# Kernel optimization log

Measured on AMD Instinct MI355X. Metric: run time of the kernel, lower is better.

Reference implementation:

```python
import jax, jax.numpy as jnp
import numpy as np

B, T, C, L = 256, 512, 128, 64  # batch, timesteps, num_classes (blank=C-1), max label len
NEG = -1e30  # finite -inf surrogate (avoids nan in grads)


def setup_inputs() -> dict:
    key = jax.random.key(0)
    k1, k2, k3, k4 = jax.random.split(key, 4)
    logits = jax.random.normal(k1, (B, T, C), dtype=jnp.float32)
    y_pred = jax.nn.softmax(logits, axis=-1)  # ctc_batch_cost expects softmax probs
    y_true = jax.random.randint(k2, (B, L), 0, C - 1, dtype=jnp.int32)  # non-blank labels
    input_length = jax.random.randint(k3, (B, 1), T // 2, T + 1, dtype=jnp.int32)
    label_length = jax.random.randint(k4, (B, 1), L // 2, L + 1, dtype=jnp.int32)
    return {"y_true": y_true, "y_pred": y_pred,
            "input_length": input_length, "label_length": label_length}


def _ctc_loss(log_probs, labels, input_length, label_length, blank):
    # log_probs: [B,T,C]; labels: [B,L]; lengths: [B]
    b, t_max, _ = log_probs.shape
    l_max = labels.shape[1]
    s_max = 2 * l_max + 1
    # extended label sequence: blank, l1, blank, l2, ..., blank  -> [B,S]
    ext = jnp.full((b, s_max), blank, dtype=labels.dtype)
    ext = ext.at[:, 1::2].set(labels)
    # gathered log probs per extended symbol: [B,T,S]
    lp = jnp.take_along_axis(log_probs, ext[:, None, :].astype(jnp.int32), axis=2)
    # skip (s-2 -> s) allowed where ext[s] != blank and ext[s] != ext[s-2]
    skip = jnp.zeros((b, s_max), dtype=bool)
    skip = skip.at[:, 2:].set((ext[:, 2:] != blank) & (ext[:, 2:] != ext[:, :-2]))
    # init alpha at t=0: only s=0 (blank) and s=1 (first label) reachable
    alpha0 = jnp.full((b, s_max), NEG, dtype=log_probs.dtype)
    alpha0 = alpha0.at[:, 0].set(lp[:, 0, 0])
    alpha0 = alpha0.at[:, 1].set(lp[:, 0, 1])
    in_len = input_length

    def step(alpha, inp):
        lp_t, t = inp  # lp_t: [B,S]
        s1 = jnp.pad(alpha, ((0, 0), (1, 0)), constant_values=NEG)[:, :-1]
        s2 = jnp.pad(alpha, ((0, 0), (2, 0)), constant_values=NEG)[:, :-2]
        a = jnp.logaddexp(alpha, s1)
        a = jnp.where(skip, jnp.logaddexp(a, s2), a)
        new = a + lp_t
        new = jnp.where((t < in_len)[:, None], new, alpha)  # freeze past input_length
        return new, None

    lp_time_major = jnp.swapaxes(lp, 0, 1)  # [T,B,S]
    ts = jnp.arange(1, t_max)
    alpha, _ = jax.lax.scan(step, alpha0, (lp_time_major[1:], ts))
    lab = label_length
    idx_last = 2 * lab  # final blank position; idx_last-1 is final label position
    a_last = jnp.take_along_axis(alpha, idx_last[:, None], axis=1)[:, 0]
    a_prev = jnp.take_along_axis(alpha, (idx_last - 1)[:, None], axis=1)[:, 0]
    return -jnp.logaddexp(a_last, a_prev)  # [B]


def reference(y_true, y_pred, input_length, label_length):
    eps = 1e-7  # keras epsilon added before log
    log_probs = jnp.log(y_pred + eps)
    blank = y_pred.shape[-1] - 1  # keras ctc_batch_cost blank convention
    loss = _ctc_loss(log_probs, y_true, input_length[:, 0], label_length[:, 0], blank)
    return loss[:, None]  # [B,1], matching tf expand_dims(ctc_loss, 1)
```

## Files before the change

### kernel.cpp

```cpp
#include <hip/hip_runtime.h>


#define B_ 256
#define T_ 512
#define C_ 128
#define L_ 64
#define BLANK_ 127
#define EPSF (1e-7f)
#define CHUNK 32
#define QSTR 36
#define LN2F 0.6931471805599453f

#define EXP2(x) __builtin_amdgcn_exp2f(x)
#define LOG2(x) __builtin_amdgcn_logf(x)

__device__ __forceinline__ float lse2_2(float a, float b) {
    float m = fmaxf(a, b);
    float d = fminf(a, b) - m;
    return m + LOG2(1.0f + EXP2(d));
}

__device__ __forceinline__ float dppf(float x) {
    return __int_as_float(__builtin_amdgcn_update_dpp(
        0, __float_as_int(x), 0x138, 0xf, 0xf, false));
}
__device__ __forceinline__ int dppi(int x) {
    return __builtin_amdgcn_update_dpp(0, x, 0x138, 0xf, 0xf, false);
}

__device__ __forceinline__ void stage_chunk(const float* gsrc, float* ldst, int lane) {
#pragma unroll
    for (int i = 0; i < CHUNK / 2; ++i) {
        __builtin_amdgcn_global_load_lds(
            (const __attribute__((address_space(1))) void*)(gsrc + i * 256 + lane * 4),
            (__attribute__((address_space(3))) void*)(ldst + i * 256),
            16, 0, 0);
    }
}

__device__ __forceinline__ void produce_chunk(const float* __restrict__ rk,
        float* __restrict__ qd, int lane, int label, int t0, int tend, float& llg)
{
    const float pbv  = rk[(lane & 31) * C_ + BLANK_] + EPSF;
    const float rpb  = 0.5f / pbv;
    const float erpb = EPSF * rpb;
    const int t = t0 + lane;
    const bool lgv = (lane < 32) && (t >= 1) && (t < tend);
    llg += lgv ? LOG2(pbv) : 0.0f;
#pragma unroll
    for (int k = 0; k < 8; ++k) {
        float q[4];
#pragma unroll
        for (int j = 0; j < 4; ++j) {
            const int r = 4 * k + j;
            const float pl = rk[r * C_ + label];
            const float rb = __int_as_float(
                __builtin_amdgcn_readlane(__float_as_int(rpb), r));
            const float eb = __int_as_float(
                __builtin_amdgcn_readlane(__float_as_int(erpb), r));
            q[j] = fmaf(pl, rb, eb);
        }
        *reinterpret_cast<float4*>(qd + lane * QSTR + 4 * k) =
            make_float4(q[0], q[1], q[2], q[3]);
    }
}

template<bool HAS128>
__device__ __forceinline__ void maybe_renorm(float& A0, float& A1, float& A2,
                                             int& e, float& sch) {
    float m2 = fmaxf(A0, A1);
    if (HAS128) m2 = fmaxf(m2, A2);
    const bool out = (m2 > 16777216.0f) ||
                     ((m2 < 5.9604644775390625e-8f) && (m2 > 0.0f));
    if (__any(out)) {
        const float mm = (m2 == 0.0f) ? 1.0f : m2;
        const int eb = __float_as_int(mm) >> 23;
        const float s = __int_as_float((254 - eb) << 23);
        A0 *= s; A1 *= s;
        if (HAS128) A2 *= s;
        e += eb - 127;
        const int ep = dppi(e);
        int d = ep - e;
        d = d < -125 ? -125 : d;
        d = d > 127 ? 127 : d;
        sch = __int_as_float((d + 126) << 23);
    }
}

template<bool HAS128>
__device__ __forceinline__ void step(float& A0, float& A1, float& A2,
                                     float sch, float skipf2, float ql) {
    const float P1 = dppf(A1) * sch;
    const float A0o = A0, A1o = A1;
    A0 = fmaf(A0o, 0.5f, P1);
    const float t = fmaf(skipf2, P1, A0o);
    A1 = (A1o + t) * ql;
    if (HAS128) A2 = (A2 + A1o) * 0.5f;
}

template<bool HAS128>
__device__ __forceinline__ void consumer(const float (*qlbuf)[64 * QSTR],
        const float* extra, int lane, int label, int lab, int tend, int nmax,
        float* out, int b)
{
    const int lprev = __shfl_up(label, 1);
    const float skipf2 = (lane > 0 && label != lprev) ? 2.0f : 0.0f;

    float A0 = 0.0f, A1 = 0.0f, A2 = 0.0f, sch = 0.5f;
    int e = 0;

    for (int c = 0; c < nmax; ++c) {
        const float* qb = &qlbuf[c & 1][lane * QSTR];
        float qlv[32];
#pragma unroll
        for (int k = 0; k < 8; ++k) {
            const float4 t4 = *reinterpret_cast<const float4*>(qb + 4 * k);
            qlv[4*k+0] = t4.x; qlv[4*k+1] = t4.y;
            qlv[4*k+2] = t4.z; qlv[4*k+3] = t4.w;
        }
        asm volatile("s_waitcnt lgkmcnt(0)" ::: "memory");
        __builtin_amdgcn_s_barrier();
        __builtin_amdgcn_sched_barrier(0);

        const int rem = tend - c * CHUNK;
        if (c == 0) {
            A0 = (lane == 0) ? extra[1] : 0.0f;
            A1 = (lane == 0) ? extra[0] : 0.0f;
#pragma unroll
            for (int u = 1; u < 32; ++u) {
                step<HAS128>(A0, A1, A2, sch, skipf2, qlv[u]);
                if ((u & 3) == 3) maybe_renorm<HAS128>(A0, A1, A2, e, sch);
            }
        } else if (rem >= CHUNK) {
#pragma unroll
            for (int u = 0; u < 32; ++u) {
                step<HAS128>(A0, A1, A2, sch, skipf2, qlv[u]);
                if ((u & 3) == 3) maybe_renorm<HAS128>(A0, A1, A2, e, sch);
            }
        } else {
            for (int u = 0; u < rem; ++u) {
                step<HAS128>(A0, A1, A2, sch, skipf2, qlv[u]);
                if ((u & 3) == 3) maybe_renorm<HAS128>(A0, A1, A2, e, sch);
            }
        }
    }
    __builtin_amdgcn_s_barrier();
    const float lg = extra[2];
    const float ef = (float)e + lg + (float)(tend - 1);
    const float l0 = LOG2(A0) + ef;
    const float l1 = LOG2(A1) + ef;
    const float a_prev = __shfl(l1, lab - 1);
    float a_last;
    if (HAS128) {
        const float l2 = LOG2(A2) + ef;
        a_last = __shfl(l2, 63);
    } else {
        a_last = __shfl(l0, lab);
    }
    if (lane == 0) out[b] = -LN2F * lse2_2(a_last, a_prev);
}

__global__ __launch_bounds__(128) void ctc_fwd_kernel(
    const int* __restrict__ y_true, const float* __restrict__ y_pred,
    const int* __restrict__ input_len, const int* __restrict__ label_len,
    float* __restrict__ out)
{
    __shared__ __align__(16) float raw[2][CHUNK * C_];
    __shared__ __align__(16) float qlbuf[2][64 * QSTR];
    __shared__ float extra[4];

    const int b = blockIdx.x;
    const int tid = threadIdx.x;
    const int lane = tid & 63;
    const float* __restrict__ Pg = y_pred + (size_t)b * T_ * C_;
    const int label = y_true[b * L_ + lane];
    const int in_len = input_len[b];
    const int tend = in_len < T_ ? in_len : T_;
    const int nmax = (tend + CHUNK - 1) / CHUNK;

    if (tid >= 64) {
        float llg = 0.0f;
        stage_chunk(Pg, &raw[0][0], lane);
        stage_chunk(Pg + CHUNK * C_, &raw[1][0], lane);
        asm volatile("s_waitcnt vmcnt(16)" ::: "memory");
        produce_chunk(&raw[0][0], &qlbuf[0][0], lane, label, 0, tend, llg);
        if (lane == 0) {
            extra[0] = raw[0][label] + EPSF;
            extra[1] = raw[0][BLANK_] + EPSF;
        }
        asm volatile("s_waitcnt lgkmcnt(0)" ::: "memory");
        __builtin_amdgcn_s_barrier();
        for (int c = 0; c < nmax; ++c) {
            if (c + 2 < nmax)
                stage_chunk(Pg + (size_t)(c + 2) * CHUNK * C_, &raw[c & 1][0], lane);
            if (c + 1 < nmax) {
                if (c + 2 < nmax) asm volatile("s_waitcnt vmcnt(16)" ::: "memory");
                else              asm volatile("s_waitcnt vmcnt(0)" ::: "memory");
                produce_chunk(&raw[(c + 1) & 1][0], &qlbuf[(c + 1) & 1][0],
                              lane, label, (c + 1) * CHUNK, tend, llg);
            }
            asm volatile("s_waitcnt lgkmcnt(0)" ::: "memory");
            __builtin_amdgcn_s_barrier();
        }
#pragma unroll
        for (int off = 16; off >= 1; off >>= 1) llg += __shfl_xor(llg, off);
        if (lane == 0) extra[2] = llg;
        asm volatile("s_waitcnt lgkmcnt(0)" ::: "memory");
        __builtin_amdgcn_s_barrier();
    } else {
        const int lab = label_len[b];
        __builtin_amdgcn_s_barrier();
        if (lab == L_) consumer<true >(qlbuf, extra, lane, label, lab, tend, nmax, out, b);
        else           consumer<false>(qlbuf, extra, lane, label, lab, tend, nmax, out, b);
    }
}

extern "C" void kernel_launch(void* const* d_in, const int* in_sizes, int n_in,
                              void* d_out, int out_size, void* d_ws, size_t ws_size,
                              hipStream_t stream) {
    const int*   y_true    = (const int*)d_in[0];
    const float* y_pred    = (const float*)d_in[1];
    const int*   input_len = (const int*)d_in[2];
    const int*   label_len = (const int*)d_in[3];
    float* out = (float*)d_out;

    ctc_fwd_kernel<<<B_, 128, 0, stream>>>(y_true, y_pred, input_len, label_len, out);
}
```

Before: 24.33 us.

## Split CTC recursion into concurrent forward-alpha and backward-beta halves

Each batch block now runs four waves: a forward producer and consumer computing alpha over the first half of the time steps, and a backward producer and consumer computing beta over the second half. The halves are joined by a log-sum-exp of alpha times beta across lanes. This halves the serial recurrence length, which is the latency-bound critical path per block. In exchange it doubles the waves and LDS per block, adds a reverse-time data layout and a combine step, and risks numerical or indexing errors at the split point and in the backward renormalisation.

```diff
diff --git a/kernel.cpp b/kernel.cpp
--- a/kernel.cpp
+++ b/kernel.cpp
@@ -8,8 +8,10 @@
 #define BLANK_ 127
 #define EPSF (1e-7f)
 #define CHUNK 32
-#define QSTR 36
+#define QSTRF 36
+#define QSTRB 68
 #define LN2F 0.6931471805599453f
+#define NEGF (-1e30f)
 
 #define EXP2(x) __builtin_amdgcn_exp2f(x)
 #define LOG2(x) __builtin_amdgcn_logf(x)
@@ -19,16 +21,25 @@
     float d = fminf(a, b) - m;
     return m + LOG2(1.0f + EXP2(d));
 }
-
-__device__ __forceinline__ float dppf(float x) {
+__device__ __forceinline__ float dppf_shr(float x) {
     return __int_as_float(__builtin_amdgcn_update_dpp(
         0, __float_as_int(x), 0x138, 0xf, 0xf, false));
 }
-__device__ __forceinline__ int dppi(int x) {
+__device__ __forceinline__ int dppi_shr(int x) {
     return __builtin_amdgcn_update_dpp(0, x, 0x138, 0xf, 0xf, false);
 }
-
-__device__ __forceinline__ void stage_chunk(const float* gsrc, float* ldst, int lane) {
+__device__ __forceinline__ float dppf_shl(float x) {
+    return __int_as_float(__builtin_amdgcn_update_dpp(
+        0, __float_as_int(x), 0x130, 0xf, 0xf, false));
+}
+__device__ __forceinline__ int dppi_shl(int x) {
+    return __builtin_amdgcn_update_dpp(0, x, 0x130, 0xf, 0xf, false);
+}
+__device__ __forceinline__ float rdlanef(float x, int i) {
+    return __int_as_float(__builtin_amdgcn_readlane(__float_as_int(x), i));
+}
+
+__device__ __forceinline__ void stage_rows(const float* gsrc, float* ldst, int lane) {
 #pragma unroll
     for (int i = 0; i < CHUNK / 2; ++i) {
         __builtin_amdgcn_global_load_lds(
@@ -38,15 +49,14 @@
     }
 }
 
-__device__ __forceinline__ void produce_chunk(const float* __restrict__ rk,
-        float* __restrict__ qd, int lane, int label, int t0, int tend, float& llg)
+__device__ __forceinline__ void produce_fwd(const float* __restrict__ rk,
+        float* __restrict__ qd, int lane, int label, int t0, int tendF, float& llg)
 {
-    const float pbv  = rk[(lane & 31) * C_ + BLANK_] + EPSF;
-    const float rpb  = 0.5f / pbv;
-    const float erpb = EPSF * rpb;
+    const float pbv = rk[(lane & 31) * C_ + BLANK_] + EPSF;
+    const float rpb = __builtin_amdgcn_rcpf(pbv) * 0.5f;
+    const float erb = EPSF * rpb;
     const int t = t0 + lane;
-    const bool lgv = (lane < 32) && (t >= 1) && (t < tend);
-    llg += lgv ? LOG2(pbv) : 0.0f;
+    llg += ((lane < 32) && (t >= 1) && (t < tendF)) ? LOG2(pbv) : 0.0f;
 #pragma unroll
     for (int k = 0; k < 8; ++k) {
         float q[4];
@@ -54,20 +64,45 @@
         for (int j = 0; j < 4; ++j) {
             const int r = 4 * k + j;
             const float pl = rk[r * C_ + label];
-            const float rb = __int_as_float(
-                __builtin_amdgcn_readlane(__float_as_int(rpb), r));
-            const float eb = __int_as_float(
-                __builtin_amdgcn_readlane(__float_as_int(erpb), r));
-            q[j] = fmaf(pl, rb, eb);
-        }
-        *reinterpret_cast<float4*>(qd + lane * QSTR + 4 * k) =
+            q[j] = fmaf(pl, rdlanef(rpb, r), rdlanef(erb, r));
+        }
+        *reinterpret_cast<float4*>(qd + lane * QSTRF + 4 * k) =
             make_float4(q[0], q[1], q[2], q[3]);
     }
 }
 
+__device__ __forceinline__ void produce_bwd(const float* __restrict__ rk,
+        float* __restrict__ qd, int lane, int label, float kf,
+        int tLo, int start, float& llg)
+{
+    const float pbv = rk[(lane & 31) * C_ + BLANK_] + EPSF;
+    const float rpb = __builtin_amdgcn_rcpf(pbv) * 0.5f;
+    const float erb = EPSF * rpb;
+    const int t = start + (lane & 31);
+    llg += ((lane < 32) && (t >= tLo)) ? LOG2(pbv) : 0.0f;
+    float* base = qd + lane * QSTRB;
+#pragma unroll
+    for (int k = 0; k < 8; ++k) {
+        float q4[4], k4[4];
+#pragma unroll
+        for (int j = 0; j < 4; ++j) {
+            const int r = 4 * k + j;
+            const float pl = rk[r * C_ + label];
+            const float qv = fmaf(pl, rdlanef(rpb, r), rdlanef(erb, r));
+            float ksh = __shfl_down(kf * qv, 1);
+            k4[j] = (lane < 63) ? ksh : 0.0f;
+            q4[j] = qv;
+        }
+        *reinterpret_cast<float4*>(base + (28 - 4 * k)) =
+            make_float4(q4[3], q4[2], q4[1], q4[0]);
+        *reinterpret_cast<float4*>(base + 32 + (28 - 4 * k)) =
+            make_float4(k4[3], k4[2], k4[1], k4[0]);
+    }
+}
+
 template<bool HAS128>
-__device__ __forceinline__ void maybe_renorm(float& A0, float& A1, float& A2,
-                                             int& e, float& sch) {
+__device__ __forceinline__ void renorm_f(float& A0, float& A1, float& A2,
+        int& e, float& sch, float& kq, float skipf2) {
     float m2 = fmaxf(A0, A1);
     if (HAS128) m2 = fmaxf(m2, A2);
     const bool out = (m2 > 16777216.0f) ||
@@ -79,127 +114,111 @@
         A0 *= s; A1 *= s;
         if (HAS128) A2 *= s;
         e += eb - 127;
-        const int ep = dppi(e);
-        int d = ep - e;
-        d = d < -125 ? -125 : d;
-        d = d > 127 ? 127 : d;
+        int d = dppi_shr(e) - e;
+        d = d < -125 ? -125 : (d > 127 ? 127 : d);
         sch = __int_as_float((d + 126) << 23);
-    }
-}
-
+        kq = skipf2 * sch;
+    }
+}
 template<bool HAS128>
-__device__ __forceinline__ void step(float& A0, float& A1, float& A2,
-                                     float sch, float skipf2, float ql) {
-    const float P1 = dppf(A1) * sch;
+__device__ __forceinline__ void step_f(float& A0, float& A1, float& A2,
+        float sch, float kq, float ql) {
+    const float P1 = dppf_shr(A1) * sch;
     const float A0o = A0, A1o = A1;
     A0 = fmaf(A0o, 0.5f, P1);
-    const float t = fmaf(skipf2, P1, A0o);
-    A1 = (A1o + t) * ql;
+    const float t = fmaf(kq, dppf_shr(A1o), A0o);
+    A1 = (A1o + fmaf(kq, 0.0f, t - A0o + A0o)) * ql;
     if (HAS128) A2 = (A2 + A1o) * 0.5f;
 }
 
+
 template<bool HAS128>
-__device__ __forceinline__ void consumer(const float (*qlbuf)[64 * QSTR],
-        const float* extra, int lane, int label, int lab, int tend, int nmax,
-        float* out, int b)
-{
-    const int lprev = __shfl_up(label, 1);
-    const float skipf2 = (lane > 0 && label != lprev) ? 2.0f : 0.0f;
-
-    float A0 = 0.0f, A1 = 0.0f, A2 = 0.0f, sch = 0.5f;
-    int e = 0;
-
-    for (int c = 0; c < nmax; ++c) {
-        const float* qb = &qlbuf[c & 1][lane * QSTR];
-        float qlv[32];
-#pragma unroll
-        for (int k = 0; k < 8; ++k) {
-            const float4 t4 = *reinterpret_cast<const float4*>(qb + 4 * k);
-            qlv[4*k+0] = t4.x; qlv[4*k+1] = t4.y;
-            qlv[4*k+2] = t4.z; qlv[4*k+3] = t4.w;
-        }
-        asm volatile("s_waitcnt lgkmcnt(0)" ::: "memory");
-        __builtin_amdgcn_s_barrier();
-        __builtin_amdgcn_sched_barrier(0);
-
-        const int rem = tend - c * CHUNK;
-        if (c == 0) {
-            A0 = (lane == 0) ? extra[1] : 0.0f;
-            A1 = (lane == 0) ? extra[0] : 0.0f;
-#pragma unroll
-            for (int u = 1; u < 32; ++u) {
-                step<HAS128>(A0, A1, A2, sch, skipf2, qlv[u]);
-                if ((u & 3) == 3) maybe_renorm<HAS128>(A0, A1, A2, e, sch);
-            }
-        } else if (rem >= CHUNK) {
-#pragma unroll
-            for (int u = 0; u < 32; ++u) {
-                step<HAS128>(A0, A1, A2, sch, skipf2, qlv[u]);
-                if ((u & 3) == 3) maybe_renorm<HAS128>(A0, A1, A2, e, sch);
-            }
-        } else {
-            for (int u = 0; u < rem; ++u) {
-                step<HAS128>(A0, A1, A2, sch, skipf2, qlv[u]);
-                if ((u & 3) == 3) maybe_renorm<HAS128>(A0, A1, A2, e, sch);
-            }
-        }
-    }
-    __builtin_amdgcn_s_barrier();
-    const float lg = extra[2];
-    const float ef = (float)e + lg + (float)(tend - 1);
-    const float l0 = LOG2(A0) + ef;
-    const float l1 = LOG2(A1) + ef;
-    const float a_prev = __shfl(l1, lab - 1);
-    float a_last;
-    if (HAS128) {
-        const float l2 = LOG2(A2) + ef;
-        a_last = __shfl(l2, 63);
-    } else {
-        a_last = __shfl(l0, lab);
-    }
-    if (lane == 0) out[b] = -LN2F * lse2_2(a_last, a_prev);
-}
-
-__global__ __launch_bounds__(128) void ctc_fwd_kernel(
+__device__ __forceinline__ void renorm_b(float& b0, float& b1, float& b2,
+        int& e, float& schB, float& scfB) {
+    float m2 = fmaxf(b0, b1);
+    if (HAS128) m2 = fmaxf(m2, b2);
+    const bool out = (m2 > 16777216.0f) ||
+                     ((m2 < 5.9604644775390625e-8f) && (m2 > 0.0f));
+    if (__any(out)) {
+        const float mm = (m2 == 0.0f) ? 1.0f : m2;
+        const int eb = __float_as_int(mm) >> 23;
+        const float s = __int_as_float((254 - eb) << 23);
+        b0 *= s; b1 *= s;
+        if (HAS128) b2 *= s;
+        e += eb - 127;
+        int d = dppi_shl(e) - e;
+        d = d < -125 ? -125 : (d > 126 ? 126 : d);
+        scfB = __int_as_float((d + 127) << 23);
+        schB = __int_as_float((d + 126) << 23);
+    }
+}
+template<bool HAS128>
+__device__ __forceinline__ void step_b(float& b0, float& b1, float& b2,
+        float schB, float scfB, float h63, float q, float ksh) {
+    const float s0 = dppf_shl(b0);
+    const float s1 = dppf_shl(b1);
+    const float t1 = q * b1;
+    const float b0n = fmaf(0.5f, b0, t1);
+    float t2 = fmaf(schB, s0, t1);
+    if (HAS128) t2 = fmaf(h63, b2, t2);
+    const float b1n = fmaf(scfB, ksh * s1, t2);
+    if (HAS128) b2 *= 0.5f;
+    b0 = b0n; b1 = b1n;
+}
+
+__global__ __launch_bounds__(256) void ctc_fwd_kernel(
     const int* __restrict__ y_true, const float* __restrict__ y_pred,
     const int* __restrict__ input_len, const int* __restrict__ label_len,
     float* __restrict__ out)
 {
-    __shared__ __align__(16) float raw[2][CHUNK * C_];
-    __shared__ __align__(16) float qlbuf[2][64 * QSTR];
-    __shared__ float extra[4];
+    __shared__ __align__(16) float rawF[2][CHUNK * C_];
+    __shared__ __align__(16) float rawB[2][CHUNK * C_];
+    __shared__ __align__(16) float qf[2][64 * QSTRF];
+    __shared__ __align__(16) float qb[2][64 * QSTRB];
+    __shared__ float bstate[4][64];
+    __shared__ float extra[8];
 
     const int b = blockIdx.x;
     const int tid = threadIdx.x;
     const int lane = tid & 63;
+    const int wid = tid >> 6;
     const float* __restrict__ Pg = y_pred + (size_t)b * T_ * C_;
     const int label = y_true[b * L_ + lane];
     const int in_len = input_len[b];
     const int tend = in_len < T_ ? in_len : T_;
-    const int nmax = (tend + CHUNK - 1) / CHUNK;
-
-    if (tid >= 64) {
+    const int m_ = (tend - 1) >> 1;
+    const int tendF = m_ + 1;
+    const int mB = tend - 1 - m_;
+    const int nf = (tendF + CHUNK - 1) / CHUNK;
+    const int nb = (mB + CHUNK - 1) / CHUNK;
+    const int NI = nf;
+    const int lprev = __shfl_up(label, 1);
+    const float kf = (lane > 0 && label != lprev) ? 1.0f : 0.0f;
+    const int lab = label_len[b];
+    const bool has128 = (lab == L_);
+
+    if (wid == 2) {
         float llg = 0.0f;
-        stage_chunk(Pg, &raw[0][0], lane);
-        stage_chunk(Pg + CHUNK * C_, &raw[1][0], lane);
+        stage_rows(Pg, rawF[0], lane);
+        stage_rows(Pg + CHUNK * C_, rawF[1], lane);
         asm volatile("s_waitcnt vmcnt(16)" ::: "memory");
-        produce_chunk(&raw[0][0], &qlbuf[0][0], lane, label, 0, tend, llg);
+        produce_fwd(rawF[0], qf[0], lane, label, 0, tendF, llg);
         if (lane == 0) {
-            extra[0] = raw[0][label] + EPSF;
-            extra[1] = raw[0][BLANK_] + EPSF;
+            extra[0] = rawF[0][label]  + EPSF;
+            extra[1] = rawF[0][BLANK_] + EPSF;
         }
         asm volatile("s_waitcnt lgkmcnt(0)" ::: "memory");
         __builtin_amdgcn_s_barrier();
-        for (int c = 0; c < nmax; ++c) {
-            if (c + 2 < nmax)
-                stage_chunk(Pg + (size_t)(c + 2) * CHUNK * C_, &raw[c & 1][0], lane);
-            if (c + 1 < nmax) {
-                if (c + 2 < nmax) asm volatile("s_waitcnt vmcnt(16)" ::: "memory");
-                else              asm volatile("s_waitcnt vmcnt(0)" ::: "memory");
-                produce_chunk(&raw[(c + 1) & 1][0], &qlbuf[(c + 1) & 1][0],
-                              lane, label, (c + 1) * CHUNK, tend, llg);
-            }
-            asm volatile("s_waitcnt lgkmcnt(0)" ::: "memory");
+        for (int i = 0; i < NI; ++i) {
+            if (i + 2 < nf)
+                stage_rows(Pg + (size_t)(i + 2) * CHUNK * C_, rawF[i & 1], lane);
+            if (i + 1 < nf) {
+                if (i + 2 < nf) asm volatile("s_waitcnt vmcnt(16)" ::: "memory");
+                else            asm volatile("s_waitcnt vmcnt(0)" ::: "memory");
+                produce_fwd(rawF[(i + 1) & 1], qf[(i + 1) & 1], lane, label,
+                            (i + 1) * CHUNK, tendF, llg);
+                asm volatile("s_waitcnt lgkmcnt(0)" ::: "memory");
+            }
             __builtin_amdgcn_s_barrier();
         }
 #pragma unroll
@@ -207,11 +226,202 @@
         if (lane == 0) extra[2] = llg;
         asm volatile("s_waitcnt lgkmcnt(0)" ::: "memory");
         __builtin_amdgcn_s_barrier();
+    } else if (wid == 3) {
+        float llg = 0.0f;
+        stage_rows(Pg + (size_t)(tend - CHUNK) * C_, rawB[0], lane);
+        stage_rows(Pg + (size_t)(tend - 2 * CHUNK) * C_, rawB[1], lane);
+        asm volatile("s_waitcnt vmcnt(16)" ::: "memory");
+        produce_bwd(rawB[0], qb[0], lane, label, kf, tendF, tend - CHUNK, llg);
+        asm volatile("s_waitcnt lgkmcnt(0)" ::: "memory");
+        __builtin_amdgcn_s_barrier();
+        for (int i = 0; i < NI; ++i) {
+            if (i + 2 < nb)
+                stage_rows(Pg + (size_t)(tend - (i + 3) * CHUNK) * C_,
+                           rawB[i & 1], lane);
+            if (i + 1 < nb) {
+                if (i + 2 < nb) asm volatile("s_waitcnt vmcnt(16)" ::: "memory");
+                else            asm volatile("s_waitcnt vmcnt(0)" ::: "memory");
+                produce_bwd(rawB[(i + 1) & 1], qb[(i + 1) & 1], lane, label, kf,
+                            tendF, tend - (i + 2) * CHUNK, llg);
+                asm volatile("s_waitcnt lgkmcnt(0)" ::: "memory");
+            }
+            __builtin_amdgcn_s_barrier();
+        }
+#pragma unroll
+        for (int off = 16; off >= 1; off >>= 1) llg += __shfl_xor(llg, off);
+        if (lane == 0) extra[3] = llg;
+        asm volatile("s_waitcnt lgkmcnt(0)" ::: "memory");
+        __builtin_amdgcn_s_barrier();
+    } else if (wid == 1) {
+        const float h63 = (lane == 63) ? 0.5f : 0.0f;
+        float b0 = (!has128 && lane == lab) ? 1.0f : 0.0f;
+        float b1 = (lane == lab - 1) ? 1.0f : 0.0f;
+        float b2 = (has128 && lane == 63) ? 1.0f : 0.0f;
+        float schB = 0.5f, scfB = 1.0f;
+        int e = 0;
+        __builtin_amdgcn_s_barrier();
+        for (int d = 0; d < NI; ++d) {
+            if (d < nb) {
+                const float* qp = &qb[d & 1][lane * QSTRB];
+                float q[CHUNK], ks[CHUNK];
+#pragma unroll
+                for (int k = 0; k < 8; ++k) {
+                    const float4 t4 = *reinterpret_cast<const float4*>(qp + 4 * k);
+                    q[4*k+0] = t4.x; q[4*k+1] = t4.y; q[4*k+2] = t4.z; q[4*k+3] = t4.w;
+                }
+#pragma unroll
+                for (int k = 0; k < 8; ++k) {
+                    const float4 t4 = *reinterpret_cast<const float4*>(qp + 32 + 4 * k);
+                    ks[4*k+0] = t4.x; ks[4*k+1] = t4.y; ks[4*k+2] = t4.z; ks[4*k+3] = t4.w;
+                }
+                asm volatile("s_waitcnt lgkmcnt(0)" ::: "memory");
+                __builtin_amdgcn_s_barrier();
+                __builtin_amdgcn_sched_barrier(0);
+                const int len = mB - d * CHUNK;
+                if (has128) {
+                    if (len >= CHUNK) {
+#pragma unroll
+                        for (int u = 0; u < CHUNK; ++u) {
+                            step_b<true>(b0, b1, b2, schB, scfB, h63, q[u], ks[u]);
+                            if ((u & 3) == 3) renorm_b<true>(b0, b1, b2, e, schB, scfB);
+                        }
+                    } else {
+#pragma unroll
+                        for (int u = 0; u < CHUNK; ++u) {
+                            const float o0 = b0, o1 = b1, o2 = b2;
+                            step_b<true>(b0, b1, b2, schB, scfB, h63, q[u], ks[u]);
+                            const bool v = u < len;
+                            b0 = v ? b0 : o0; b1 = v ? b1 : o1; b2 = v ? b2 : o2;
+                            if ((u & 3) == 3) renorm_b<true>(b0, b1, b2, e, schB, scfB);
+                        }
+                    }
+                } else {
+                    if (len >= CHUNK) {
+#pragma unroll
+                        for (int u = 0; u < CHUNK; ++u) {
+                            step_b<false>(b0, b1, b2, schB, scfB, h63, q[u], ks[u]);
+                            if ((u & 3) == 3) renorm_b<false>(b0, b1, b2, e, schB, scfB);
+                        }
+                    } else {
+#pragma unroll
+                        for (int u = 0; u < CHUNK; ++u) {
+                            const float o0 = b0, o1 = b1;
+                            step_b<false>(b0, b1, b2, schB, scfB, h63, q[u], ks[u]);
+                            const bool v = u < len;
+                            b0 = v ? b0 : o0; b1 = v ? b1 : o1;
+                            if ((u & 3) == 3) renorm_b<false>(b0, b1, b2, e, schB, scfB);
+                        }
+                    }
+                }
+            } else {
+                __builtin_amdgcn_s_barrier();
+            }
+        }
+        bstate[0][lane] = b0;
+        bstate[1][lane] = b1;
+        bstate[2][lane] = b2;
+        bstate[3][lane] = (float)e;
+        asm volatile("s_waitcnt lgkmcnt(0)" ::: "memory");
+        __builtin_amdgcn_s_barrier();
     } else {
-        const int lab = label_len[b];
-        __builtin_amdgcn_s_barrier();
-        if (lab == L_) consumer<true >(qlbuf, extra, lane, label, lab, tend, nmax, out, b);
-        else           consumer<false>(qlbuf, extra, lane, label, lab, tend, nmax, out, b);
+        const float skipf2 = 2.0f * kf;
+        float A0 = 0.0f, A1 = 0.0f, A2 = 0.0f;
+        float sch = 0.5f, kq = skipf2 * 0.5f;
+        int e = 0;
+        __builtin_amdgcn_s_barrier();
+        for (int c = 0; c < NI; ++c) {
+            const float* qp = &qf[c & 1][lane * QSTRF];
+            float q[CHUNK];
+#pragma unroll
+            for (int k = 0; k < 8; ++k) {
+                const float4 t4 = *reinterpret_cast<const float4*>(qp + 4 * k);
+                q[4*k+0] = t4.x; q[4*k+1] = t4.y; q[4*k+2] = t4.z; q[4*k+3] = t4.w;
+            }
+            asm volatile("s_waitcnt lgkmcnt(0)" ::: "memory");
+            __builtin_amdgcn_s_barrier();
+            __builtin_amdgcn_sched_barrier(0);
+            const int rem = tendF - c * CHUNK;
+            const int u0 = (c == 0) ? 1 : 0;
+            if (c == 0) {
+                A0 = (lane == 0) ? extra[1] : 0.0f;
+                A1 = (lane == 0) ? extra[0] : 0.0f;
+            }
+            if (has128) {
+                if (rem >= CHUNK) {
+#pragma unroll
+                    for (int u = 0; u < CHUNK; ++u) {
+                        if (u >= u0) {
+                            const float P1 = dppf_shr(A1) * sch;
+                            const float A0o = A0, A1o = A1;
+                            A0 = fmaf(A0o, 0.5f, P1);
+                            const float t = fmaf(skipf2, P1, A0o);
+                            A1 = (A1o + t) * q[u];
+                            A2 = (A2 + A1o) * 0.5f;
+                        }
+                        if ((u & 3) == 3) renorm_f<true>(A0, A1, A2, e, sch, kq, skipf2);
+                    }
+                } else {
+#pragma unroll
+                    for (int u = 0; u < CHUNK; ++u) {
+                        const float o0 = A0, o1 = A1, o2 = A2;
+                        const float P1 = dppf_shr(A1) * sch;
+                        A0 = fmaf(o0, 0.5f, P1);
+                        const float t = fmaf(skipf2, P1, o0);
+                        A1 = (o1 + t) * q[u];
+                        A2 = (A2 + o1) * 0.5f;
+                        const bool v = u < rem;
+                        A0 = v ? A0 : o0; A1 = v ? A1 : o1; A2 = v ? A2 : o2;
+                        if ((u & 3) == 3) renorm_f<true>(A0, A1, A2, e, sch, kq, skipf2);
+                    }
+                }
+            } else {
+                if (rem >= CHUNK) {
+#pragma unroll
+                    for (int u = 0; u < CHUNK; ++u) {
+                        if (u >= u0) {
+                            const float P1 = dppf_shr(A1) * sch;
+                            const float A0o = A0, A1o = A1;
+                            A0 = fmaf(A0o, 0.5f, P1);
+                            const float t = fmaf(skipf2, P1, A0o);
+                            A1 = (A1o + t) * q[u];
+                        }
+                        if ((u & 3) == 3) renorm_f<false>(A0, A1, A2, e, sch, kq, skipf2);
+                    }
+                } else {
+#pragma unroll
+                    for (int u = 0; u < CHUNK; ++u) {
+                        const float o0 = A0, o1 = A1;
+                        const float P1 = dppf_shr(A1) * sch;
+                        A0 = fmaf(o0, 0.5f, P1);
+                        const float t = fmaf(skipf2, P1, o0);
+                        A1 = (o1 + t) * q[u];
+                        const bool v = u < rem;
+                        A0 = v ? A0 : o0; A1 = v ? A1 : o1;
+                        if ((u & 3) == 3) renorm_f<false>(A0, A1, A2, e, sch, kq, skipf2);
+                    }
+                }
+            }
+        }
+        __builtin_amdgcn_s_barrier();
+        const float B0v = bstate[0][lane];
+        const float B1v = bstate[1][lane];
+        const float B2v = bstate[2][lane];
+        const float es  = (float)e + bstate[3][lane];
+        float l0 = LOG2(A0) + LOG2(B0v) + es;
+        float l1 = LOG2(A1) + LOG2(B1v) + es;
+        l0 = fmaxf(l0, NEGF);
+        l1 = fmaxf(l1, NEGF);
+        float v = lse2_2(l0, l1);
+        if (has128) {
+            float l2 = LOG2(A2) + LOG2(B2v) + es;
+            l2 = (lane == 63) ? fmaxf(l2, NEGF) : NEGF;
+            v = lse2_2(v, l2);
+        }
+#pragma unroll
+        for (int off = 32; off >= 1; off >>= 1)
+            v = lse2_2(v, __shfl_xor(v, off));
+        if (lane == 0)
+            out[b] = -LN2F * (v + extra[2] + extra[3] + (float)(tend - 1));
     }
 }
 
@@ -224,5 +434,5 @@
     const int*   label_len = (const int*)d_in[3];
     float* out = (float*)d_out;
 
-    ctc_fwd_kernel<<<B_, 128, 0, stream>>>(y_true, y_pred, input_len, label_len, out);
-}
+    ctc_fwd_kernel<<<B_, 256, 0, stream>>>(y_true, y_pred, input_len, label_len, out);
+}
```

New measurement: 24.17 us. About the same (-0.7%).
